# Optimization experiments

Measured on AMD Instinct MI355X. Metric: run time of the kernel, lower is better.

The kernel has to match this reference:

```python
import jax, jax.numpy as jnp
import numpy as np

IN_F = 1024
HID_F = 4096
OUT_F = 1024
B = 64
D = 768
SPARSE_RATIO = 0.1


def setup_inputs() -> dict:
    key = jax.random.key(0)
    k_x, k_w1, k_w2, k_b, k_m = jax.random.split(key, 5)
    # x: [batch, tokens(d), in_features(s)]
    x = jax.random.normal(k_x, (B, D, IN_F), dtype=jnp.float32)
    # scale weights like typical init so GELU inputs stay in a sane range
    fc1_w = jax.random.normal(k_w1, (HID_F, IN_F), dtype=jnp.float32) * (1.0 / np.sqrt(IN_F))
    fc2_w = jax.random.normal(k_w2, (OUT_F, HID_F), dtype=jnp.float32) * (1.0 / np.sqrt(HID_F))
    fc2_b = jax.random.normal(k_b, (OUT_F,), dtype=jnp.float32) * 0.02
    sparse_mask = (jax.random.uniform(k_m, (IN_F, OUT_F)) < SPARSE_RATIO).astype(jnp.float32)
    return {"x": x, "fc1_w": fc1_w, "fc2_w": fc2_w, "fc2_b": fc2_b, "sparse_mask": sparse_mask}


def reference(x, fc1_w, fc2_w, fc2_b, sparse_mask):
    # attn_s[s,t] = sum_d fc1_w[d,s] * fc2_w[t,d] + fc2_b[t]   -> [in, out]
    attn = (jnp.einsum('ds,td->st', fc1_w, fc2_w) + fc2_b) * sparse_mask
    # dropout with p=0.0 is the identity
    out = jnp.einsum('bds,st->bdt', x, attn)  # [B, D, out]
    # torch nn.GELU default is the exact (erf) variant
    return jax.nn.gelu(out, approximate=False)
```

## Files before the change

### kernel.cpp

```cpp
#include <hip/hip_runtime.h>
#include <hip/hip_bf16.h>
#include <math.h>

typedef __attribute__((ext_vector_type(8))) short  short8;
typedef __attribute__((ext_vector_type(4))) float  floatx4;
typedef __attribute__((ext_vector_type(4))) int    i32x4;

__device__ __forceinline__ ushort f2bf(float f) {
    __hip_bfloat16 hb = __float2bfloat16(f);
    return *(ushort*)&hb;
}
__device__ __forceinline__ short8 pack8(float4 a, float4 b) {
    union { short8 v; ushort u[8]; } r;
    r.u[0] = f2bf(a.x); r.u[1] = f2bf(a.y); r.u[2] = f2bf(a.z); r.u[3] = f2bf(a.w);
    r.u[4] = f2bf(b.x); r.u[5] = f2bf(b.y); r.u[6] = f2bf(b.z); r.u[7] = f2bf(b.w);
    return r.v;
}

typedef __attribute__((address_space(1))) const void* gas1_t;
typedef __attribute__((address_space(3))) void*       las3_t;
__device__ __forceinline__ void gload16(const void* g, void* l) {
    __builtin_amdgcn_global_load_lds((gas1_t)g, (las3_t)l, 16, 0, 0);
}
__device__ __forceinline__ short8 ds_read16(uint off) {
    union { i32x4 i; short8 s; } u;
    asm volatile("ds_read_b128 %0, %1" : "=v"(u.i) : "v"(off));
    return u.s;
}

__global__ __launch_bounds__(256) void k_cvt(const float* __restrict__ in,
                                             ushort* __restrict__ out, int n8) {
    int i = blockIdx.x * 256 + threadIdx.x;
    if (i >= n8) return;
    const float4* p = reinterpret_cast<const float4*>(in) + (size_t)i * 2;
    float4 a = p[0], b = p[1];
    *reinterpret_cast<short8*>(out + (size_t)i * 8) = pack8(a, b);
}

__global__ __launch_bounds__(256) void k_transpose(const float* __restrict__ in,
                                                   ushort* __restrict__ out) {
    __shared__ float sm[64][65];
    const int tid = threadIdx.x;
    const int s0 = blockIdx.x * 64;
    const int d0 = blockIdx.y * 64;
#pragma unroll
    for (int i = 0; i < 4; ++i) {
        int lin = i * 256 + tid;
        int dr  = lin >> 4;
        int sc4 = lin & 15;
        float4 v = *reinterpret_cast<const float4*>(&in[(size_t)(d0 + dr) * 1024 + s0 + sc4 * 4]);
        sm[dr][sc4 * 4 + 0] = v.x; sm[dr][sc4 * 4 + 1] = v.y;
        sm[dr][sc4 * 4 + 2] = v.z; sm[dr][sc4 * 4 + 3] = v.w;
    }
    __syncthreads();
#pragma unroll
    for (int i = 0; i < 8; ++i) {
        int lin = i * 256 + tid;
        int dc2 = lin & 31;
        int sr  = lin >> 5;
        uint lo = (uint)f2bf(sm[dc2 * 2][sr]);
        uint hi = (uint)f2bf(sm[dc2 * 2 + 1][sr]);
        *reinterpret_cast<uint*>(&out[(size_t)(s0 + sr) * 4096 + d0 + dc2 * 2]) = lo | (hi << 16);
    }
}

template <int BM, int BN, int EPI, int SWZ>
__global__ __launch_bounds__(256) void k_gemm_b(const ushort* __restrict__ A,
                                                const ushort* __restrict__ B,
                                                const float* __restrict__ bias,
                                                const float* __restrict__ mask,
                                                void* __restrict__ Cout,
                                                int lda, int ldb, int ksteps) {
    __shared__ ushort As[BM * 32];
    __shared__ ushort Bs[BN * 32];
    const int tid  = threadIdx.x;
    const int wave = tid >> 6, lane = tid & 63;
    const int wm = wave >> 1, wn = wave & 1;
    const int quad = lane >> 4, m16 = lane & 15;

    if (EPI == 2) {
        const int sp = blockIdx.z;
        A += (size_t)sp * 1024;
        B += (size_t)sp * 1024;
        Cout = (void*)((float*)Cout + (size_t)sp * 1048576);
    }

    int bx = blockIdx.x, by = blockIdx.y;
    if (SWZ) {
        const int nx   = gridDim.x;
        const int nwg  = nx * gridDim.y;
        const int orig = by * nx + bx;
        const int cpx  = nwg >> 3;
        const int w    = (orig & 7) * cpx + (orig >> 3);
        bx = w % nx; by = w / nx;
    }
    const int n0 = bx * BN;
    const int m0 = by * BM;

    constexpr int AI = BM / 32;
    constexpr int BJ = BN / 32;
    floatx4 acc[AI][BJ];
    const floatx4 zero = {0.f, 0.f, 0.f, 0.f};
#pragma unroll
    for (int i = 0; i < AI; ++i)
#pragma unroll
        for (int j = 0; j < BJ; ++j) acc[i][j] = zero;

    const int gr = lane >> 2;
    const int gc = (lane & 3) * 8;

    for (int kt = 0; kt < ksteps; ++kt) {
        const int k0 = kt * 32;
        if (kt) __syncthreads();
#pragma unroll
        for (int t = 0; t < BM / 64; ++t) {
            const int r = wave * (BM / 4) + t * 16;
            gload16(&A[(size_t)(m0 + r + gr) * lda + k0 + gc], &As[r * 32]);
        }
#pragma unroll
        for (int t = 0; t < BN / 64; ++t) {
            const int r = wave * (BN / 4) + t * 16;
            gload16(&B[(size_t)(n0 + r + gr) * ldb + k0 + gc], &Bs[r * 32]);
        }
        __syncthreads();

        short8 aF[AI], bF[BJ];
#pragma unroll
        for (int i = 0; i < AI; ++i)
            aF[i] = *reinterpret_cast<const short8*>(&As[(wm * (BM / 2) + i * 16 + m16) * 32 + quad * 8]);
#pragma unroll
        for (int j = 0; j < BJ; ++j)
            bF[j] = *reinterpret_cast<const short8*>(&Bs[(wn * (BN / 2) + j * 16 + m16) * 32 + quad * 8]);
#pragma unroll
        for (int i = 0; i < AI; ++i)
#pragma unroll
            for (int j = 0; j < BJ; ++j)
                acc[i][j] = __builtin_amdgcn_mfma_f32_16x16x32_bf16(aF[i], bF[j], acc[i][j], 0, 0, 0);
    }

#pragma unroll
    for (int i = 0; i < AI; ++i) {
#pragma unroll
        for (int j = 0; j < BJ; ++j) {
            const int col = n0 + wn * (BN / 2) + j * 16 + m16;
            float bv = 0.f;
            if (EPI == 0) bv = bias[col];
#pragma unroll
            for (int rr = 0; rr < 4; ++rr) {
                const int row = m0 + wm * (BM / 2) + i * 16 + quad * 4 + rr;
                float v = acc[i][j][rr];
                if (EPI == 0) {
                    v = (v + bv) * mask[(size_t)row * 1024 + col];
                    ((ushort*)Cout)[(size_t)col * 1024 + row] = f2bf(v);
                } else if (EPI == 1) {
                    float g = 0.5f * v * (1.0f + erff(v * 0.70710678118654752f));
                    ((float*)Cout)[(size_t)row * 1024 + col] = g;
                } else {
                    ((float*)Cout)[(size_t)col * 1024 + row] = v;
                }
            }
        }
    }
}

__global__ __launch_bounds__(256) void k_attn_fin(const float* __restrict__ P,
                                                  const float* __restrict__ bias,
                                                  const float* __restrict__ mask,
                                                  ushort* __restrict__ attnT) {
    const int idx = blockIdx.x * 256 + threadIdx.x;
    const int t  = idx >> 7;
    const int s0 = (idx & 127) << 3;
    float s[8];
#pragma unroll
    for (int j = 0; j < 8; ++j) s[j] = 0.f;
#pragma unroll
    for (int sp = 0; sp < 4; ++sp) {
        const float4* p = reinterpret_cast<const float4*>(&P[(size_t)sp * 1048576 + (size_t)t * 1024 + s0]);
        float4 a = p[0], b = p[1];
        s[0] += a.x; s[1] += a.y; s[2] += a.z; s[3] += a.w;
        s[4] += b.x; s[5] += b.y; s[6] += b.z; s[7] += b.w;
    }
    const float bv = bias[t];
    union { short8 v; ushort u[8]; } r;
#pragma unroll
    for (int j = 0; j < 8; ++j) {
        float v = (s[j] + bv) * mask[(size_t)(s0 + j) * 1024 + t];
        r.u[j] = f2bf(v);
    }
    *reinterpret_cast<short8*>(&attnT[(size_t)t * 1024 + s0]) = r.v;
}

#define GPH(T_, C_, KS_, MH_, RDB_, NB_)                                         \
  do {                                                                           \
    _Pragma("unroll")                                                            \
    for (int i_ = 0; i_ < 4; ++i_)                                               \
      aA[i_] = ds_read16(bA_ + (uint)((KS_) * 16384 + ((MH_) * 4 + i_) * 1024)); \
    if (RDB_) {                                                                  \
      _Pragma("unroll")                                                          \
      for (int j_ = 0; j_ < 4; ++j_)                                             \
        bB[j_] = ds_read16(bB_ + (uint)((KS_) * 16384 + j_ * 1024));             \
    }                                                                            \
    stage_ht(4 * (T_) + (C_) + 5);                                               \
    __builtin_amdgcn_sched_barrier(0);                                           \
    __builtin_amdgcn_s_barrier();                                                \
    asm volatile("s_waitcnt lgkmcnt(0)");                                        \
    __builtin_amdgcn_sched_barrier(0);                                           \
    __builtin_amdgcn_s_setprio(1);                                               \
    _Pragma("unroll")                                                            \
    for (int i_ = 0; i_ < 4; ++i_) {                                             \
      _Pragma("unroll")                                                          \
      for (int j_ = 0; j_ < 4; ++j_)                                             \
        acc[(MH_) * 4 + i_][j_] = __builtin_amdgcn_mfma_f32_16x16x32_bf16(       \
            aA[i_], bB[j_], acc[(MH_) * 4 + i_][j_], 0, 0, 0);                   \
    }                                                                            \
    __builtin_amdgcn_s_setprio(0);                                               \
    __builtin_amdgcn_sched_barrier(0);                                           \
    if ((NB_) >= 0) {                                                            \
      if ((NB_) == 4) asm volatile("s_waitcnt vmcnt(4)");                        \
      else            asm volatile("s_waitcnt vmcnt(0)");                        \
      __builtin_amdgcn_sched_barrier(0);                                         \
    }                                                                            \
    __builtin_amdgcn_s_barrier();                                                \
    __builtin_amdgcn_sched_barrier(0);                                           \
  } while (0)

__global__ __launch_bounds__(512) void k_gemm8(const ushort* __restrict__ A,
                                               const ushort* __restrict__ B,
                                               float* __restrict__ C) {
    constexpr int NT = 16;
    __shared__ __align__(16) ushort lds[65536];

    const int tid  = threadIdx.x;
    const int wave = tid >> 6, lane = tid & 63;
    const int wm = wave >> 2, wn = wave & 3;
    const int quad = lane >> 4, m16 = lane & 15;

    const int orig = blockIdx.y * 4 + blockIdx.x;
    const int wsz  = (orig & 7) * 96 + (orig >> 3);
    const int n0 = (wsz & 3) * 256;
    const int m0 = (wsz >> 2) * 256;

    const uint lds0 = (uint)(size_t)(las3_t)(void*)lds;
    const uint xorM = (uint)((m16 & 6) << 3);
    const uint baseA = lds0 + ((((uint)(wm * 128 + m16)) * 64u + (uint)quad * 16u) ^ xorM);
    const uint baseB = lds0 + 32768u + ((((uint)(wn * 64 + m16)) * 64u + (uint)quad * 16u) ^ xorM);

    const int srow   = lane >> 2;
    const int schunk = (((lane & 3) ^ ((lane >> 3) & 3)) << 3);

    auto stage_ht = [&](int g) {
        if (g >= 4 * NT) return;
        const int tg = g >> 2, ig = g & 3;
        const int mat = ig & 1, ks = ig >> 1;
        const int kc  = tg * 64 + ks * 32 + schunk;
        const uint dst0 = (uint)(((tg & 1) << 16) | (mat << 15) | (ks << 14));
        const ushort* src = mat ? B : A;
        const int r0 = (mat ? n0 : m0) + srow;
#pragma unroll
        for (int e = 0; e < 2; ++e) {
            const int s = e * 8 + wave;
            gload16(&src[(size_t)(r0 + s * 16) * 1024 + kc],
                    (void*)((char*)lds + dst0 + (uint)(s << 10)));
        }
    };

    floatx4 acc[8][4];
    const floatx4 zf = {0.f, 0.f, 0.f, 0.f};
#pragma unroll
    for (int i = 0; i < 8; ++i)
#pragma unroll
        for (int j = 0; j < 4; ++j) acc[i][j] = zf;
    short8 aA[4], bB[4];

#pragma unroll
    for (int g = 0; g < 6; ++g) stage_ht(g);
    asm volatile("s_waitcnt vmcnt(4)");
    __builtin_amdgcn_sched_barrier(0);
    __builtin_amdgcn_s_barrier();
    __builtin_amdgcn_sched_barrier(0);

    for (int tp = 0; tp < NT / 2; ++tp) {
        const int t0 = 2 * tp, t1 = 2 * tp + 1;
        {
            const uint bA_ = baseA, bB_ = baseB;
            GPH(t0, 1, 0, 0, 1, -1);
            GPH(t0, 2, 0, 1, 0, -1);
            GPH(t0, 3, 1, 0, 1, -1);
            GPH(t0, 4, 1, 1, 0, (tp < 7) ? 4 : 0);
        }
        {
            const uint bA_ = baseA + 65536u, bB_ = baseB + 65536u;
            GPH(t1, 1, 0, 0, 1, -1);
            GPH(t1, 2, 0, 1, 0, -1);
            GPH(t1, 3, 1, 0, 1, -1);
            GPH(t1, 4, 1, 1, 0, (tp < 7) ? 4 : -1);
        }
    }

#pragma unroll
    for (int mf = 0; mf < 8; ++mf) {
#pragma unroll
        for (int nf = 0; nf < 4; ++nf) {
            const int col = n0 + wn * 64 + nf * 16 + m16;
#pragma unroll
            for (int rr = 0; rr < 4; ++rr) {
                const int row = m0 + wm * 128 + mf * 16 + quad * 4 + rr;
                const float v = acc[mf][nf][rr];
                C[(size_t)row * 1024 + col] = 0.5f * v * (1.0f + erff(v * 0.70710678118654752f));
            }
        }
    }
}

__global__ __launch_bounds__(256) void k_gemm_f32a(const float* __restrict__ Af,
                                                   const ushort* __restrict__ B,
                                                   float* __restrict__ Cout,
                                                   int lda, int ldb, int ksteps) {
    __shared__ ushort As[128 * 32];
    __shared__ ushort Bs[128 * 32];
    const int tid  = threadIdx.x;
    const int wave = tid >> 6, lane = tid & 63;
    const int wm = wave >> 1, wn = wave & 1;
    const int quad = lane >> 4, m16 = lane & 15;
    const int n0 = blockIdx.x * 128;
    const int m0 = blockIdx.y * 128;

    floatx4 acc[4][4];
    const floatx4 zero = {0.f, 0.f, 0.f, 0.f};
#pragma unroll
    for (int i = 0; i < 4; ++i)
#pragma unroll
        for (int j = 0; j < 4; ++j) acc[i][j] = zero;

    const int s_r = tid >> 2;
    const int s_c = tid & 3;
    const int gr = lane >> 2;
    const int gc = (lane & 3) * 8;

    for (int kt = 0; kt < ksteps; ++kt) {
        const int k0 = kt * 32;
        const float* r0 = &Af[(size_t)(m0 + s_r) * lda + k0 + s_c * 8];
        const float* r1 = &Af[(size_t)(m0 + 64 + s_r) * lda + k0 + s_c * 8];
        short8 a0 = pack8(*reinterpret_cast<const float4*>(r0), *reinterpret_cast<const float4*>(r0 + 4));
        short8 a1 = pack8(*reinterpret_cast<const float4*>(r1), *reinterpret_cast<const float4*>(r1 + 4));
        __syncthreads();
        *reinterpret_cast<short8*>(&As[(s_r)      * 32 + s_c * 8]) = a0;
        *reinterpret_cast<short8*>(&As[(64 + s_r) * 32 + s_c * 8]) = a1;
#pragma unroll
        for (int t = 0; t < 2; ++t) {
            const int r = wave * 32 + t * 16;
            gload16(&B[(size_t)(n0 + r + gr) * ldb + k0 + gc], &Bs[r * 32]);
        }
        __syncthreads();

        short8 aF[4], bF[4];
#pragma unroll
        for (int i = 0; i < 4; ++i)
            aF[i] = *reinterpret_cast<const short8*>(&As[(wm * 64 + i * 16 + m16) * 32 + quad * 8]);
#pragma unroll
        for (int j = 0; j < 4; ++j)
            bF[j] = *reinterpret_cast<const short8*>(&Bs[(wn * 64 + j * 16 + m16) * 32 + quad * 8]);
#pragma unroll
        for (int i = 0; i < 4; ++i)
#pragma unroll
            for (int j = 0; j < 4; ++j)
                acc[i][j] = __builtin_amdgcn_mfma_f32_16x16x32_bf16(aF[i], bF[j], acc[i][j], 0, 0, 0);
    }

#pragma unroll
    for (int i = 0; i < 4; ++i)
#pragma unroll
        for (int j = 0; j < 4; ++j) {
            const int col = n0 + wn * 64 + j * 16 + m16;
#pragma unroll
            for (int rr = 0; rr < 4; ++rr) {
                const int row = m0 + wm * 64 + i * 16 + quad * 4 + rr;
                float v = acc[i][j][rr];
                Cout[(size_t)row * 1024 + col] = 0.5f * v * (1.0f + erff(v * 0.70710678118654752f));
            }
        }
}

extern "C" void kernel_launch(void* const* d_in, const int* in_sizes, int n_in,
                              void* d_out, int out_size, void* d_ws, size_t ws_size,
                              hipStream_t stream) {
    const float* x    = (const float*)d_in[0];
    const float* fc1w = (const float*)d_in[1];
    const float* fc2w = (const float*)d_in[2];
    const float* fc2b = (const float*)d_in[3];
    const float* mask = (const float*)d_in[4];

    char* ws = (char*)d_ws;
    ushort* fc1T  = (ushort*)ws;
    ushort* fc2wb = (ushort*)(ws + (8u  << 20));
    ushort* attnT = (ushort*)(ws + (16u << 20));
    float*  attnP = (float*)(ws + (18u << 20));
    ushort* xb    = (ushort*)(ws + (18u << 20));
    const size_t XB_BYTES = 50331648ull * 2;
    const bool has_xb = ws_size >= (size_t)(18u << 20) + XB_BYTES;
    const bool has_p  = ws_size >= (size_t)(34u << 20);

    k_transpose<<<dim3(16, 64), 256, 0, stream>>>(fc1w, fc1T);
    k_cvt<<<2048, 256, 0, stream>>>(fc2w, fc2wb, 524288);

    if (has_p) {
        k_gemm_b<64, 64, 2, 1><<<dim3(16, 16, 4), 256, 0, stream>>>(
            fc1T, fc2wb, nullptr, nullptr, attnP, 4096, 4096, 32);
        k_attn_fin<<<512, 256, 0, stream>>>(attnP, fc2b, mask, attnT);
    } else {
        k_gemm_b<64, 64, 0, 1><<<dim3(16, 16), 256, 0, stream>>>(
            fc1T, fc2wb, fc2b, mask, attnT, 4096, 4096, 128);
    }

    if (has_xb) {
        k_cvt<<<24576, 256, 0, stream>>>(x, xb, 6291456);
        k_gemm8<<<dim3(4, 192), 512, 0, stream>>>(xb, attnT, (float*)d_out);
    } else {
        k_gemm_f32a<<<dim3(8, 384), 256, 0, stream>>>(x, attnT, (float*)d_out, 1024, 1024, 32);
    }
}
```

Baseline: 509.3 us.

## Double-buffer LDS fragment reads in main GEMM and coalesce attn finalize

New measurement: 550.5 us. 8.1% more time.

```diff
diff --git a/kernel.cpp b/kernel.cpp
--- a/kernel.cpp
+++ b/kernel.cpp
@@ -152,11 +152,8 @@
                 if (EPI == 0) {
                     v = (v + bv) * mask[(size_t)row * 1024 + col];
                     ((ushort*)Cout)[(size_t)col * 1024 + row] = f2bf(v);
-                } else if (EPI == 1) {
-                    float g = 0.5f * v * (1.0f + erff(v * 0.70710678118654752f));
-                    ((float*)Cout)[(size_t)row * 1024 + col] = g;
                 } else {
-                    ((float*)Cout)[(size_t)col * 1024 + row] = v;
+                    ((float*)Cout)[(size_t)row * 1024 + col] = v;
                 }
             }
         }
@@ -167,62 +164,80 @@
                                                   const float* __restrict__ bias,
                                                   const float* __restrict__ mask,
                                                   ushort* __restrict__ attnT) {
-    const int idx = blockIdx.x * 256 + threadIdx.x;
-    const int t  = idx >> 7;
-    const int s0 = (idx & 127) << 3;
-    float s[8];
-#pragma unroll
-    for (int j = 0; j < 8; ++j) s[j] = 0.f;
-#pragma unroll
-    for (int sp = 0; sp < 4; ++sp) {
-        const float4* p = reinterpret_cast<const float4*>(&P[(size_t)sp * 1048576 + (size_t)t * 1024 + s0]);
-        float4 a = p[0], b = p[1];
-        s[0] += a.x; s[1] += a.y; s[2] += a.z; s[3] += a.w;
-        s[4] += b.x; s[5] += b.y; s[6] += b.z; s[7] += b.w;
-    }
-    const float bv = bias[t];
-    union { short8 v; ushort u[8]; } r;
-#pragma unroll
-    for (int j = 0; j < 8; ++j) {
-        float v = (s[j] + bv) * mask[(size_t)(s0 + j) * 1024 + t];
-        r.u[j] = f2bf(v);
-    }
-    *reinterpret_cast<short8*>(&attnT[(size_t)t * 1024 + s0]) = r.v;
-}
-
-#define GPH(T_, C_, KS_, MH_, RDB_, NB_)                                         \
-  do {                                                                           \
-    _Pragma("unroll")                                                            \
-    for (int i_ = 0; i_ < 4; ++i_)                                               \
-      aA[i_] = ds_read16(bA_ + (uint)((KS_) * 16384 + ((MH_) * 4 + i_) * 1024)); \
-    if (RDB_) {                                                                  \
-      _Pragma("unroll")                                                          \
-      for (int j_ = 0; j_ < 4; ++j_)                                             \
-        bB[j_] = ds_read16(bB_ + (uint)((KS_) * 16384 + j_ * 1024));             \
-    }                                                                            \
-    stage_ht(4 * (T_) + (C_) + 5);                                               \
-    __builtin_amdgcn_sched_barrier(0);                                           \
-    __builtin_amdgcn_s_barrier();                                                \
-    asm volatile("s_waitcnt lgkmcnt(0)");                                        \
-    __builtin_amdgcn_sched_barrier(0);                                           \
-    __builtin_amdgcn_s_setprio(1);                                               \
-    _Pragma("unroll")                                                            \
-    for (int i_ = 0; i_ < 4; ++i_) {                                             \
-      _Pragma("unroll")                                                          \
-      for (int j_ = 0; j_ < 4; ++j_)                                             \
-        acc[(MH_) * 4 + i_][j_] = __builtin_amdgcn_mfma_f32_16x16x32_bf16(       \
-            aA[i_], bB[j_], acc[(MH_) * 4 + i_][j_], 0, 0, 0);                   \
-    }                                                                            \
-    __builtin_amdgcn_s_setprio(0);                                               \
-    __builtin_amdgcn_sched_barrier(0);                                           \
-    if ((NB_) >= 0) {                                                            \
-      if ((NB_) == 4) asm volatile("s_waitcnt vmcnt(4)");                        \
-      else            asm volatile("s_waitcnt vmcnt(0)");                        \
-      __builtin_amdgcn_sched_barrier(0);                                         \
-    }                                                                            \
-    __builtin_amdgcn_s_barrier();                                                \
-    __builtin_amdgcn_sched_barrier(0);                                           \
-  } while (0)
+    __shared__ float sm[64][65];
+    const int tid = threadIdx.x;
+    const int s0 = blockIdx.x * 64;
+    const int t0 = blockIdx.y * 64;
+#pragma unroll
+    for (int i = 0; i < 4; ++i) {
+        int lin = i * 256 + tid;
+        int sr  = lin >> 4;
+        int tc4 = lin & 15;
+        const size_t off = (size_t)(s0 + sr) * 1024 + t0 + tc4 * 4;
+        float4 acc4 = *reinterpret_cast<const float4*>(&P[off]);
+#pragma unroll
+        for (int sp = 1; sp < 4; ++sp) {
+            float4 v = *reinterpret_cast<const float4*>(&P[(size_t)sp * 1048576 + off]);
+            acc4.x += v.x; acc4.y += v.y; acc4.z += v.z; acc4.w += v.w;
+        }
+        float4 bv = *reinterpret_cast<const float4*>(&bias[t0 + tc4 * 4]);
+        float4 mk = *reinterpret_cast<const float4*>(&mask[(size_t)(s0 + sr) * 1024 + t0 + tc4 * 4]);
+        sm[sr][tc4 * 4 + 0] = (acc4.x + bv.x) * mk.x;
+        sm[sr][tc4 * 4 + 1] = (acc4.y + bv.y) * mk.y;
+        sm[sr][tc4 * 4 + 2] = (acc4.z + bv.z) * mk.z;
+        sm[sr][tc4 * 4 + 3] = (acc4.w + bv.w) * mk.w;
+    }
+    __syncthreads();
+#pragma unroll
+    for (int i = 0; i < 8; ++i) {
+        int lin = i * 256 + tid;
+        int sc2 = lin & 31;
+        int tr  = lin >> 5;
+        uint lo = (uint)f2bf(sm[sc2 * 2][tr]);
+        uint hi = (uint)f2bf(sm[sc2 * 2 + 1][tr]);
+        *reinterpret_cast<uint*>(&attnT[(size_t)(t0 + tr) * 1024 + s0 + sc2 * 2]) = lo | (hi << 16);
+    }
+}
+
+#define SB __builtin_amdgcn_sched_barrier(0)
+#define BAR __builtin_amdgcn_s_barrier()
+#define LGKM(n) asm volatile("s_waitcnt lgkmcnt(" #n ")")
+#define VMC(n)  asm volatile("s_waitcnt vmcnt(" #n ")")
+
+#define RD_A(dst_, base_, ks_, mh_)                                             \
+  { _Pragma("unroll")                                                           \
+    for (int i_ = 0; i_ < 4; ++i_)                                              \
+      dst_[i_] = ds_read16((base_) + (uint)((ks_)*16384 + ((mh_)*4 + i_)*1024)); }
+#define RD_B(dst_, base_, ks_)                                                  \
+  { _Pragma("unroll")                                                           \
+    for (int j_ = 0; j_ < 4; ++j_)                                              \
+      dst_[j_] = ds_read16((base_) + (uint)((ks_)*16384 + j_*1024)); }
+#define MFMA16(aS_, bS_, MH_)                                                   \
+  { __builtin_amdgcn_s_setprio(1);                                              \
+    _Pragma("unroll")                                                           \
+    for (int i_ = 0; i_ < 4; ++i_) {                                            \
+      _Pragma("unroll")                                                         \
+      for (int j_ = 0; j_ < 4; ++j_)                                            \
+        acc[(MH_)*4 + i_][j_] = __builtin_amdgcn_mfma_f32_16x16x32_bf16(        \
+            aS_[i_], bS_[j_], acc[(MH_)*4 + i_][j_], 0, 0, 0);                  \
+    }                                                                           \
+    __builtin_amdgcn_s_setprio(0); SB; }
+
+#define BODY1(T_, bA_, bB_)                                                     \
+  stage_ht(4*(T_) + 7); RD_A(a1, bA_, 0, 1);                                    \
+  SB; BAR; SB; LGKM(4); SB; MFMA16(a0, b0, 0)
+#define BODY2(T_, bA_, bB_)                                                     \
+  stage_ht(4*(T_) + 8); RD_A(a0, bA_, 1, 0); RD_B(b1, bB_, 1);                  \
+  SB; BAR; SB; LGKM(8); SB; MFMA16(a1, b0, 1)
+#define BODY3(T_, bA_, bB_)                                                     \
+  stage_ht(4*(T_) + 9); RD_A(a1, bA_, 1, 1);                                    \
+  SB; BAR; SB; LGKM(4); SB; MFMA16(a0, b1, 0)
+#define BODY4(T_, nA_, nB_, G_)                                                 \
+  stage_ht(4*(T_) + 10); SB; VMC(G_); SB; BAR; SB;                              \
+  RD_A(a0, nA_, 0, 0); RD_B(b0, nB_, 0);                                        \
+  SB; LGKM(8); SB; MFMA16(a1, b1, 1)
+#define BODY4F()                                                                \
+  SB; BAR; SB; LGKM(0); SB; MFMA16(a1, b1, 1)
 
 __global__ __launch_bounds__(512) void k_gemm8(const ushort* __restrict__ A,
                                                const ushort* __restrict__ B,
@@ -270,31 +285,30 @@
     for (int i = 0; i < 8; ++i)
 #pragma unroll
         for (int j = 0; j < 4; ++j) acc[i][j] = zf;
-    short8 aA[4], bB[4];
-
-#pragma unroll
-    for (int g = 0; g < 6; ++g) stage_ht(g);
-    asm volatile("s_waitcnt vmcnt(4)");
-    __builtin_amdgcn_sched_barrier(0);
-    __builtin_amdgcn_s_barrier();
-    __builtin_amdgcn_sched_barrier(0);
-
-    for (int tp = 0; tp < NT / 2; ++tp) {
+    short8 a0[4], a1[4], b0[4], b1[4];
+
+#pragma unroll
+    for (int g = 0; g < 7; ++g) stage_ht(g);
+    SB; VMC(6); SB; BAR; SB;
+    RD_A(a0, baseA, 0, 0);
+    RD_B(b0, baseB, 0);
+
+    for (int tp = 0; tp < 7; ++tp) {
         const int t0 = 2 * tp, t1 = 2 * tp + 1;
-        {
-            const uint bA_ = baseA, bB_ = baseB;
-            GPH(t0, 1, 0, 0, 1, -1);
-            GPH(t0, 2, 0, 1, 0, -1);
-            GPH(t0, 3, 1, 0, 1, -1);
-            GPH(t0, 4, 1, 1, 0, (tp < 7) ? 4 : 0);
-        }
-        {
-            const uint bA_ = baseA + 65536u, bB_ = baseB + 65536u;
-            GPH(t1, 1, 0, 0, 1, -1);
-            GPH(t1, 2, 0, 1, 0, -1);
-            GPH(t1, 3, 1, 0, 1, -1);
-            GPH(t1, 4, 1, 1, 0, (tp < 7) ? 4 : -1);
-        }
+        const uint cA = baseA, cB = baseB;
+        const uint dA = baseA + 65536u, dB = baseB + 65536u;
+        BODY1(t0, cA, cB); BODY2(t0, cA, cB); BODY3(t0, cA, cB);
+        BODY4(t0, dA, dB, 6);
+        BODY1(t1, dA, dB); BODY2(t1, dA, dB); BODY3(t1, dA, dB);
+        BODY4(t1, cA, cB, 6);
+    }
+    {
+        const uint cA = baseA, cB = baseB;
+        const uint dA = baseA + 65536u, dB = baseB + 65536u;
+        BODY1(14, cA, cB); BODY2(14, cA, cB); BODY3(14, cA, cB);
+        BODY4(14, dA, dB, 0);
+        BODY1(15, dA, dB); BODY2(15, dA, dB); BODY3(15, dA, dB);
+        BODY4F();
     }
 
 #pragma unroll
@@ -406,7 +420,7 @@
     if (has_p) {
         k_gemm_b<64, 64, 2, 1><<<dim3(16, 16, 4), 256, 0, stream>>>(
             fc1T, fc2wb, nullptr, nullptr, attnP, 4096, 4096, 32);
-        k_attn_fin<<<512, 256, 0, stream>>>(attnP, fc2b, mask, attnT);
+        k_attn_fin<<<dim3(16, 16), 256, 0, stream>>>(attnP, fc2b, mask, attnT);
     } else {
         k_gemm_b<64, 64, 0, 1><<<dim3(16, 16), 256, 0, stream>>>(
             fc1T, fc2wb, fc2b, mask, attnT, 4096, 4096, 128);
```
